# Kernel tuning notes

Measured on AMD Instinct MI355X. Metric: run time of the kernel, lower is better.

The kernel has to match this reference:

```python
import jax, jax.numpy as jnp
import numpy as np

N, E, F_IN, HID, EDIM = 20000, 320000, 16, 64, 1


def _add_self_loops(src, dst, eattr, n):
    # PyG add_self_loops with fill_value='mean': self-loop edge_attr = mean of
    # incoming edge_attr per destination node (0 if no incoming edges).
    deg = jax.ops.segment_sum(jnp.ones_like(eattr[:, 0]), dst, num_segments=n)
    mean_attr = jax.ops.segment_sum(eattr, dst, num_segments=n) / jnp.maximum(deg, 1.0)[:, None]
    loop = jnp.arange(n)
    return (jnp.concatenate([src, loop]), jnp.concatenate([dst, loop]),
            jnp.concatenate([eattr, mean_attr], axis=0))


def _gat_layer(x, src, dst, eattr, W, a_src, a_dst, We, a_e, b, heads, out_ch, n):
    # shared linear for src/dst (PyG GATConv with int in_channels)
    h = (x @ W).reshape(n, heads, out_ch)                      # [N,H,C]
    al_s = jnp.einsum('nhc,hc->nh', h, a_src)                  # [N,H]
    al_d = jnp.einsum('nhc,hc->nh', h, a_dst)
    ef = (eattr @ We).reshape(-1, heads, out_ch)               # [E,H,C]
    al_e = jnp.einsum('ehc,hc->eh', ef, a_e)                   # [E,H]
    alpha = jax.nn.leaky_relu(al_s[src] + al_d[dst] + al_e, 0.2)
    # segment softmax over destination node
    m = jax.ops.segment_max(alpha, dst, num_segments=n)
    m = jnp.where(jnp.isfinite(m), m, 0.0)
    ex = jnp.exp(alpha - m[dst])
    den = jax.ops.segment_sum(ex, dst, num_segments=n)
    coef = ex / (den[dst] + 1e-16)                             # [E,H]
    out = jax.ops.segment_sum(h[src] * coef[:, :, None], dst, num_segments=n)
    return out.reshape(n, heads * out_ch) + b


def setup_inputs() -> dict:
    key = jax.random.key(0)
    ks = jax.random.split(key, 24)
    s = 0.1
    inp = {
        'x': jax.random.normal(ks[0], (N, F_IN), jnp.float32),
        'edge_index': jax.random.randint(ks[1], (2, E), 0, N, jnp.int64),
        'edge_attr': jax.random.uniform(ks[2], (E, EDIM), jnp.float32),
        # layer 0: heads=4, in=16, out=64
        'W0': jax.random.normal(ks[3], (F_IN, 4 * HID), jnp.float32) * s,
        'as0': jax.random.normal(ks[4], (4, HID), jnp.float32) * s,
        'ad0': jax.random.normal(ks[5], (4, HID), jnp.float32) * s,
        'We0': jax.random.normal(ks[6], (EDIM, 4 * HID), jnp.float32) * s,
        'ae0': jax.random.normal(ks[7], (4, HID), jnp.float32) * s,
        'b0': jnp.zeros((4 * HID,), jnp.float32),
        # layer 1: heads=4, in=256, out=64
        'W1': jax.random.normal(ks[8], (4 * HID, 4 * HID), jnp.float32) * s,
        'as1': jax.random.normal(ks[9], (4, HID), jnp.float32) * s,
        'ad1': jax.random.normal(ks[10], (4, HID), jnp.float32) * s,
        'We1': jax.random.normal(ks[11], (EDIM, 4 * HID), jnp.float32) * s,
        'ae1': jax.random.normal(ks[12], (4, HID), jnp.float32) * s,
        'b1': jnp.zeros((4 * HID,), jnp.float32),
        # layer 2: heads=1, in=256, out=64
        'W2': jax.random.normal(ks[13], (4 * HID, HID), jnp.float32) * s,
        'as2': jax.random.normal(ks[14], (1, HID), jnp.float32) * s,
        'ad2': jax.random.normal(ks[15], (1, HID), jnp.float32) * s,
        'We2': jax.random.normal(ks[16], (EDIM, HID), jnp.float32) * s,
        'ae2': jax.random.normal(ks[17], (1, HID), jnp.float32) * s,
        'b2': jnp.zeros((HID,), jnp.float32),
        'ln_g': jnp.ones((HID,), jnp.float32),
        'ln_b': jnp.zeros((HID,), jnp.float32),
    }
    return inp


def reference(x, edge_index, edge_attr,
              W0, as0, ad0, We0, ae0, b0,
              W1, as1, ad1, We1, ae1, b1,
              W2, as2, ad2, We2, ae2, b2,
              ln_g, ln_b):
    n = x.shape[0]
    src, dst, eattr = _add_self_loops(edge_index[0], edge_index[1], edge_attr, n)
    h = _gat_layer(x, src, dst, eattr, W0, as0, ad0, We0, ae0, b0, 4, HID, n)
    h = jax.nn.elu(h)  # dropout is identity in eval
    h = _gat_layer(h, src, dst, eattr, W1, as1, ad1, We1, ae1, b1, 4, HID, n)
    h = jax.nn.elu(h)
    h = _gat_layer(h, src, dst, eattr, W2, as2, ad2, We2, ae2, b2, 1, HID, n)
    mu = jnp.mean(h, axis=-1, keepdims=True)
    var = jnp.mean((h - mu) ** 2, axis=-1, keepdims=True)
    return (h - mu) / jnp.sqrt(var + 1e-5) * ln_g + ln_b
```

## Files before the change

### kernel.cpp

```cpp
#include <hip/hip_runtime.h>
#include <hip/hip_bf16.h>
#include <math.h>


typedef __attribute__((ext_vector_type(8))) short short8;
typedef __attribute__((ext_vector_type(4))) float float4v;

#define CAP 64

__device__ __forceinline__ float wave_sum(float v) {
#pragma unroll
  for (int off = 32; off > 0; off >>= 1) v += __shfl_xor(v, off, 64);
  return v;
}

__device__ __forceinline__ unsigned short f2bf(float v) {
  unsigned u = __float_as_uint(v);
  unsigned r = u + 0x7fff + ((u >> 16) & 1);
  return (unsigned short)(r >> 16);
}

__device__ __forceinline__ float bf2f(unsigned short u) {
  return __uint_as_float(((unsigned)u) << 16);
}

__device__ __forceinline__ float sel4(float a, float b, float c, float d, int i) {
  return (i == 0) ? a : (i == 1) ? b : (i == 2) ? c : d;
}

__global__ __launch_bounds__(256) void k1_kernel(
    const float* __restrict__ x, const int* __restrict__ srcv, const int* __restrict__ dstv,
    const float* __restrict__ eattr,
    const float* __restrict__ W0, const float* __restrict__ as0, const float* __restrict__ ad0,
    const float* __restrict__ We0, const float* __restrict__ ae0,
    const float* __restrict__ W1, const float* __restrict__ as1, const float* __restrict__ ad1,
    const float* __restrict__ We1, const float* __restrict__ ae1,
    const float* __restrict__ W2, const float* __restrict__ as2, const float* __restrict__ ad2,
    const float* __restrict__ We2, const float* __restrict__ ae2,
    unsigned short* __restrict__ Wf1, unsigned short* __restrict__ Wf2,
    float* __restrict__ wedot, float* __restrict__ al0s, float* __restrict__ al0d,
    int* __restrict__ deg, int2* __restrict__ ebuf,
    int N, int E, int gD) {
  int b = blockIdx.x;
  int tid = threadIdx.x;
  if (b < 272) {
    int idx = b * 256 + tid;
    int j = idx & 7, lane = (idx >> 3) & 63, ks = (idx >> 9) & 7, nt = idx >> 12;
    int k = ks * 32 + (lane >> 4) * 8 + j;
    int col = lane & 15;
    float v = 0.f;
    if (nt < 16) {
      v = W1[(size_t)k * 256 + nt * 16 + col];
    } else if (col < 4) {
      for (int c = 0; c < 64; c++) v = fmaf(W1[(size_t)k * 256 + col * 64 + c], as1[col * 64 + c], v);
    } else if (col < 8) {
      int h = col - 4;
      for (int c = 0; c < 64; c++) v = fmaf(W1[(size_t)k * 256 + h * 64 + c], ad1[h * 64 + c], v);
    }
    Wf1[idx] = f2bf(v);
  } else if (b < 352) {
    int idx = (b - 272) * 256 + tid;
    int j = idx & 7, lane = (idx >> 3) & 63, ks = (idx >> 9) & 7, nt = idx >> 12;
    int k = ks * 32 + (lane >> 4) * 8 + j;
    int col = lane & 15;
    float v = 0.f;
    if (nt < 4) {
      v = W2[(size_t)k * 64 + nt * 16 + col];
    } else if (col < 1) {
      for (int c = 0; c < 64; c++) v = fmaf(W2[(size_t)k * 64 + c], as2[c], v);
    } else if (col < 2) {
      for (int c = 0; c < 64; c++) v = fmaf(W2[(size_t)k * 64 + c], ad2[c], v);
    }
    Wf2[idx] = f2bf(v);
  } else if (b == 352) {
    if (tid >= 64) return;
    int c = tid;
    for (int h = 0; h < 4; h++) {
      float v = wave_sum(We0[h * 64 + c] * ae0[h * 64 + c]);
      if (c == 0) wedot[h] = v;
    }
    for (int h = 0; h < 4; h++) {
      float v = wave_sum(We1[h * 64 + c] * ae1[h * 64 + c]);
      if (c == 0) wedot[4 + h] = v;
    }
    float v = wave_sum(We2[c] * ae2[c]);
    if (c == 0) wedot[8] = v;
  } else if (b < 353 + gD) {
    __shared__ float va[128];
    if (tid < 128) {
      int k = tid >> 3, col = tid & 7;
      float v = 0.f;
      if (col < 4) {
        for (int c = 0; c < 64; c++) v = fmaf(W0[(size_t)k * 256 + col * 64 + c], as0[col * 64 + c], v);
      } else {
        int h = col - 4;
        for (int c = 0; c < 64; c++) v = fmaf(W0[(size_t)k * 256 + h * 64 + c], ad0[h * 64 + c], v);
      }
      va[tid] = v;
    }
    __syncthreads();
    int node = (b - 353) * 256 + tid;
    if (node >= N) return;
    const float4* xr = (const float4*)(x + (size_t)node * 16);
    float4 xv[4];
#pragma unroll
    for (int q = 0; q < 4; q++) xv[q] = xr[q];
    float al[8];
#pragma unroll
    for (int j = 0; j < 8; j++) al[j] = 0.f;
#pragma unroll
    for (int k = 0; k < 16; k++) {
      float xk = ((const float*)xv)[k];
#pragma unroll
      for (int j = 0; j < 8; j++) al[j] = fmaf(xk, va[k * 8 + j], al[j]);
    }
    ((float4*)al0s)[node] = make_float4(al[0], al[1], al[2], al[3]);
    ((float4*)al0d)[node] = make_float4(al[4], al[5], al[6], al[7]);
  } else {
    int e = (b - 353 - gD) * 256 + tid;
    if (e >= E) return;
    int d = dstv[e];
    int s = srcv[e];
    float ea = eattr[e];
    int pos = atomicAdd(&deg[d], 1);
    if (pos < CAP) ebuf[(size_t)d * CAP + pos] = make_int2(s, __float_as_int(ea));
  }
}

__global__ __launch_bounds__(256) void fused0_kernel(
    const int* __restrict__ deg, const int2* __restrict__ ebuf,
    const float* __restrict__ al0s, const float* __restrict__ al0d,
    const float* __restrict__ wedot,
    const float* __restrict__ x, const float* __restrict__ W0,
    const float* __restrict__ b0, const unsigned short* __restrict__ Wf1,
    unsigned short* __restrict__ buf256, float* __restrict__ al1s,
    float* __restrict__ al1d, int n) {
  __shared__ unsigned short hrow[16][264];
  __shared__ float w0lds[4096];
  int tile = blockIdx.x;
  int wv = threadIdx.x >> 6;
  int lane = threadIdx.x & 63;
  int es = lane >> 4;
  int c = lane & 15;
  int le = lane >> 2;
  int lh = lane & 3;

#pragma unroll
  for (int i = 0; i < 4; i++) {
    int idx = i * 256 + threadIdx.x;
    ((float4*)w0lds)[idx] = ((const float4*)W0)[idx];
  }
  __syncthreads();

  for (int s = 0; s < 4; s++) {
    int r = wv * 4 + s;
    int node = tile * 16 + r;
    if (node < n) {
      int dg = deg[node];
      int cnt = dg < CAP ? dg : CAP;
      float xself = x[(size_t)node * 16 + c];
      float4 as4s = ((const float4*)al0s)[node];
      float4 ald4 = ((const float4*)al0d)[node];
      float aldP = sel4(ald4.x, ald4.y, ald4.z, ald4.w, lh);
      float wd0 = wedot[0], wd1 = wedot[1], wd2 = wedot[2], wd3 = wedot[3];
      float wdP = sel4(wd0, wd1, wd2, wd3, lh);

      float Z[4] = {0.f, 0.f, 0.f, 0.f};
      float denP = 0.f;
      float easumP = 0.f;

      for (int i = 0; i < cnt; i += 16) {
        int slot = i + le;
        bool av = slot < cnt;
        int2 re = ebuf[(size_t)node * CAP + slot];
        int srcE = av ? re.x : 0;
        float ev = av ? __int_as_float(re.y) : 0.f;
        int srcK[4];
        float xvK[4];
#pragma unroll
        for (int k = 0; k < 4; k++) srcK[k] = __shfl(srcE, (k * 4 + es) * 4, 64);
#pragma unroll
        for (int k = 0; k < 4; k++) xvK[k] = x[(size_t)srcK[k] * 16 + c];
        float a = al0s[(size_t)srcE * 4 + lh] + aldP + ev * wdP;
        a = fmaxf(a, 0.2f * a);
        a = fminf(a, 30.f);
        float wE = av ? __expf(a) : 0.f;
        denP += wE;
        easumP += (lh == 0) ? ev : 0.f;
#pragma unroll
        for (int k = 0; k < 4; k++) {
          int e4 = (k * 4 + es) * 4;
          float w0v = __shfl(wE, e4 + 0, 64);
          float w1v = __shfl(wE, e4 + 1, 64);
          float w2v = __shfl(wE, e4 + 2, 64);
          float w3v = __shfl(wE, e4 + 3, 64);
          Z[0] = fmaf(w0v, xvK[k], Z[0]);
          Z[1] = fmaf(w1v, xvK[k], Z[1]);
          Z[2] = fmaf(w2v, xvK[k], Z[2]);
          Z[3] = fmaf(w3v, xvK[k], Z[3]);
        }
      }

#pragma unroll
      for (int h = 0; h < 4; h++) {
        Z[h] += __shfl_xor(Z[h], 16, 64);
        Z[h] += __shfl_xor(Z[h], 32, 64);
      }
      denP += __shfl_xor(denP, 4, 64);
      denP += __shfl_xor(denP, 8, 64);
      denP += __shfl_xor(denP, 16, 64);
      denP += __shfl_xor(denP, 32, 64);
      float easum = wave_sum(easumP);

      float dsel = __shfl(denP, es, 64);
      float evs = easum / fmaxf((float)dg, 1.f);
      float as_e = sel4(as4s.x, as4s.y, as4s.z, as4s.w, es);
      float ald_e = sel4(ald4.x, ald4.y, ald4.z, ald4.w, es);
      float wd_e = sel4(wd0, wd1, wd2, wd3, es);
      float aS = as_e + ald_e + evs * wd_e;
      aS = fmaxf(aS, 0.2f * aS);
      aS = fminf(aS, 30.f);
      float wvs = __expf(aS);
      dsel += wvs;
      float zsel = sel4(Z[0], Z[1], Z[2], Z[3], es) + wvs * xself;
      float zn = zsel / (dsel + 1e-16f);

      float zc[16];
      int basel = lane & 48;
#pragma unroll
      for (int cc = 0; cc < 16; cc++) zc[cc] = __shfl(zn, basel + cc, 64);
      float o[4];
      float4 b4 = ((const float4*)b0)[lane];
#pragma unroll
      for (int jj = 0; jj < 4; jj++) o[jj] = ((const float*)&b4)[jj];
#pragma unroll
      for (int cc = 0; cc < 16; cc++) {
        float4 w0r = *(const float4*)&w0lds[cc * 256 + lane * 4];
#pragma unroll
        for (int jj = 0; jj < 4; jj++) o[jj] = fmaf(zc[cc], ((const float*)&w0r)[jj], o[jj]);
      }
      ushort4 o4;
      float ox = o[0] > 0.f ? o[0] : expm1f(o[0]);
      float oy = o[1] > 0.f ? o[1] : expm1f(o[1]);
      float oz = o[2] > 0.f ? o[2] : expm1f(o[2]);
      float ow = o[3] > 0.f ? o[3] : expm1f(o[3]);
      o4.x = f2bf(ox);
      o4.y = f2bf(oy);
      o4.z = f2bf(oz);
      o4.w = f2bf(ow);
      *(ushort4*)&hrow[r][lane * 4] = o4;
    } else {
      *(ushort4*)&hrow[r][lane * 4] = make_ushort4(0, 0, 0, 0);
    }
  }
  __syncthreads();

  int m = lane & 15, q = lane >> 4;
  int row0 = tile * 16;
  short8 afrag[8];
#pragma unroll
  for (int ks = 0; ks < 8; ks++) afrag[ks] = *(short8*)&hrow[m][ks * 32 + q * 8];

  const short8* wf = (const short8*)Wf1;
  for (int nt = wv; nt < 17; nt += 4) {
    const short8* bl = wf + (size_t)nt * 8 * 64 + lane;
    short8 bf[8];
#pragma unroll
    for (int ks = 0; ks < 8; ks++) bf[ks] = bl[ks * 64];
    float4v acc = {0.f, 0.f, 0.f, 0.f};
#pragma unroll
    for (int ks = 0; ks < 8; ks++)
      acc = __builtin_amdgcn_mfma_f32_16x16x32_bf16(afrag[ks], bf[ks], acc, 0, 0, 0);
    if (nt < 16) {
      int col = nt * 16 + m;
#pragma unroll
      for (int reg = 0; reg < 4; reg++) {
        int rr = row0 + q * 4 + reg;
        if (rr < n) buf256[(size_t)rr * 256 + col] = f2bf(acc[reg]);
      }
    } else {
#pragma unroll
      for (int reg = 0; reg < 4; reg++) {
        int rr = row0 + q * 4 + reg;
        if (rr < n) {
          if (m < 4) al1s[(size_t)rr * 4 + m] = acc[reg];
          else if (m < 8) al1d[(size_t)rr * 4 + (m - 4)] = acc[reg];
        }
      }
    }
  }
}

__global__ __launch_bounds__(256) void fused1_kernel(
    const int* __restrict__ deg, const int2* __restrict__ ebuf,
    const float* __restrict__ al1s, const float* __restrict__ al1d,
    const float* __restrict__ wedot,
    const unsigned short* __restrict__ buf256, const float* __restrict__ b1,
    const unsigned short* __restrict__ Wf2, unsigned short* __restrict__ buf64,
    float* __restrict__ al2s, float* __restrict__ al2d, int n) {
  __shared__ unsigned short hrow[16][264];
  int tile = blockIdx.x;
  int wv = threadIdx.x >> 6;
  int lane = threadIdx.x & 63;
  int half = lane >> 5;
  int l = lane & 31;
  int h4 = l >> 3;
  int le = lane >> 2;
  int lh = lane & 3;
  int eA0 = half ? 1 : 0;
  int eB0 = half ? 3 : 2;

  for (int s = 0; s < 4; s++) {
    int r = wv * 4 + s;
    int node = tile * 16 + r;
    if (node < n) {
      int dg = deg[node];
      int cnt = dg < CAP ? dg : CAP;
      float aldh = al1d[(size_t)node * 4 + h4];
      float alsh = al1s[(size_t)node * 4 + h4];
      float wdh = wedot[4 + h4];
      float aldP = al1d[(size_t)node * 4 + lh];
      float wdP = wedot[4 + lh];
      short8 rowS = ((const short8*)(buf256 + (size_t)node * 256))[l];

      float acc[8];
#pragma unroll
      for (int j = 0; j < 8; j++) acc[j] = 0.f;
      float denP = 0.f;
      float easumP = 0.f;

      for (int i = 0; i < cnt; i += 16) {
        int slot = i + le;
        bool av = slot < cnt;
        int2 re = ebuf[(size_t)node * CAP + slot];
        int srcE = av ? re.x : 0;
        float ev = av ? __int_as_float(re.y) : 0.f;
        int srcA[4], srcB[4];
#pragma unroll
        for (int k = 0; k < 4; k++) {
          srcA[k] = __shfl(srcE, (k * 4 + eA0) * 4, 64);
          srcB[k] = __shfl(srcE, (k * 4 + eB0) * 4, 64);
        }
        short8 rowA[4], rowB[4];
#pragma unroll
        for (int k = 0; k < 4; k++) {
          rowA[k] = ((const short8*)(buf256 + (size_t)srcA[k] * 256))[l];
          rowB[k] = ((const short8*)(buf256 + (size_t)srcB[k] * 256))[l];
        }
        float a = al1s[(size_t)srcE * 4 + lh] + aldP + ev * wdP;
        a = fmaxf(a, 0.2f * a);
        a = fminf(a, 30.f);
        float wE = av ? __expf(a) : 0.f;
        denP += wE;
        easumP += (lh == 0) ? ev : 0.f;
#pragma unroll
        for (int k = 0; k < 4; k++) {
          float wA = __shfl(wE, (k * 4 + eA0) * 4 + h4, 64);
          float wB = __shfl(wE, (k * 4 + eB0) * 4 + h4, 64);
          const unsigned short* pa = (const unsigned short*)&rowA[k];
          const unsigned short* pb = (const unsigned short*)&rowB[k];
#pragma unroll
          for (int j = 0; j < 8; j++) acc[j] = fmaf(wA, bf2f(pa[j]), acc[j]);
#pragma unroll
          for (int j = 0; j < 8; j++) acc[j] = fmaf(wB, bf2f(pb[j]), acc[j]);
        }
      }

#pragma unroll
      for (int j = 0; j < 8; j++) acc[j] += __shfl_xor(acc[j], 32, 64);
      denP += __shfl_xor(denP, 4, 64);
      denP += __shfl_xor(denP, 8, 64);
      denP += __shfl_xor(denP, 16, 64);
      denP += __shfl_xor(denP, 32, 64);
      float easum = wave_sum(easumP);
      float den = __shfl(denP, h4, 64);

      {
        float evs = easum / fmaxf((float)dg, 1.f);
        float a = alsh + aldh + evs * wdh;
        a = fmaxf(a, 0.2f * a);
        a = fminf(a, 30.f);
        float wvv = __expf(a);
        const unsigned short* ps = (const unsigned short*)&rowS;
        den += wvv;
#pragma unroll
        for (int j = 0; j < 8; j++) acc[j] = fmaf(wvv, bf2f(ps[j]), acc[j]);
      }

      if (half == 0) {
        float inv = 1.f / (den + 1e-16f);
        float4 bb0 = ((const float4*)b1)[l * 2];
        float4 bb1 = ((const float4*)b1)[l * 2 + 1];
        unsigned short o8[8];
#pragma unroll
        for (int j = 0; j < 8; j++) {
          float bjv = (j < 4) ? ((const float*)&bb0)[j] : ((const float*)&bb1)[j - 4];
          float o = acc[j] * inv + bjv;
          o = o > 0.f ? o : expm1f(o);
          o8[j] = f2bf(o);
        }
        *(short8*)&hrow[r][l * 8] = *(short8*)o8;
      }
    } else if ((lane >> 5) == 0) {
      unsigned short z8[8] = {0, 0, 0, 0, 0, 0, 0, 0};
      *(short8*)&hrow[r][(lane & 31) * 8] = *(short8*)z8;
    }
  }
  __syncthreads();

  int m = lane & 15, q = lane >> 4;
  int row0 = tile * 16;
  short8 afrag[8];
#pragma unroll
  for (int ks = 0; ks < 8; ks++) afrag[ks] = *(short8*)&hrow[m][ks * 32 + q * 8];

  const short8* wf = (const short8*)Wf2;
  for (int nt = wv; nt < 5; nt += 4) {
    const short8* bl = wf + (size_t)nt * 8 * 64 + lane;
    short8 bf[8];
#pragma unroll
    for (int ks = 0; ks < 8; ks++) bf[ks] = bl[ks * 64];
    float4v acc = {0.f, 0.f, 0.f, 0.f};
#pragma unroll
    for (int ks = 0; ks < 8; ks++)
      acc = __builtin_amdgcn_mfma_f32_16x16x32_bf16(afrag[ks], bf[ks], acc, 0, 0, 0);
    if (nt < 4) {
      int col = nt * 16 + m;
#pragma unroll
      for (int reg = 0; reg < 4; reg++) {
        int rr = row0 + q * 4 + reg;
        if (rr < n) buf64[(size_t)rr * 64 + col] = f2bf(acc[reg]);
      }
    } else {
#pragma unroll
      for (int reg = 0; reg < 4; reg++) {
        int rr = row0 + q * 4 + reg;
        if (rr < n) {
          if (m < 1) al2s[rr] = acc[reg];
          else if (m < 2) al2d[rr] = acc[reg];
        }
      }
    }
  }
}

__global__ __launch_bounds__(256) void agg_ln_kernel(
    const int* __restrict__ deg, const int2* __restrict__ ebuf,
    const float* __restrict__ al2s, const float* __restrict__ al2d,
    const float* __restrict__ wedot,
    const unsigned short* __restrict__ B, const float* __restrict__ bias,
    const float* __restrict__ ln_g, const float* __restrict__ ln_b,
    float* __restrict__ out, int n) {
  int wv = threadIdx.x >> 6;
  int node = blockIdx.x * 4 + wv;
  if (node >= n) return;
  int lane = threadIdx.x & 63;
  int q = lane >> 4;
  int l = lane & 15;
  int le = lane & 15;
  int dg = deg[node];
  int cnt = dg < CAP ? dg : CAP;
  float ald = al2d[node];
  float als = al2s[node];
  float wd = wedot[0];
  ushort4 bvS = ((const ushort4*)(B + (size_t)node * 64))[l];

  float4 acc = make_float4(0.f, 0.f, 0.f, 0.f);
  float denP = 0.f;
  float easumP = 0.f;

  for (int i = 0; i < cnt; i += 16) {
    int slot = i + le;
    bool av = slot < cnt;
    int2 re = ebuf[(size_t)node * CAP + slot];
    int srcE = av ? re.x : 0;
    float ev = av ? __int_as_float(re.y) : 0.f;
    int srcK[4];
#pragma unroll
    for (int k = 0; k < 4; k++) srcK[k] = __shfl(srcE, k * 4 + q, 64);
    ushort4 bvK[4];
#pragma unroll
    for (int k = 0; k < 4; k++) bvK[k] = ((const ushort4*)(B + (size_t)srcK[k] * 64))[l];
    float a = al2s[srcE] + ald + ev * wd;
    a = fmaxf(a, 0.2f * a);
    a = fminf(a, 30.f);
    float wE = av ? __expf(a) : 0.f;
    denP += wE;
    easumP += ev;
#pragma unroll
    for (int k = 0; k < 4; k++) {
      float w = __shfl(wE, k * 4 + q, 64);
      acc.x = fmaf(w, bf2f(bvK[k].x), acc.x);
      acc.y = fmaf(w, bf2f(bvK[k].y), acc.y);
      acc.z = fmaf(w, bf2f(bvK[k].z), acc.z);
      acc.w = fmaf(w, bf2f(bvK[k].w), acc.w);
    }
  }

  acc.x += __shfl_xor(acc.x, 32, 64);
  acc.y += __shfl_xor(acc.y, 32, 64);
  acc.z += __shfl_xor(acc.z, 32, 64);
  acc.w += __shfl_xor(acc.w, 32, 64);
  acc.x += __shfl_xor(acc.x, 16, 64);
  acc.y += __shfl_xor(acc.y, 16, 64);
  acc.z += __shfl_xor(acc.z, 16, 64);
  acc.w += __shfl_xor(acc.w, 16, 64);
  float den = wave_sum(denP) * 0.25f;
  float easum = wave_sum(easumP) * 0.25f;

  {
    float evs = easum / fmaxf((float)dg, 1.f);
    float a = als + ald + evs * wd;
    a = fmaxf(a, 0.2f * a);
    a = fminf(a, 30.f);
    float wv2 = __expf(a);
    den += wv2;
    acc.x = fmaf(wv2, bf2f(bvS.x), acc.x);
    acc.y = fmaf(wv2, bf2f(bvS.y), acc.y);
    acc.z = fmaf(wv2, bf2f(bvS.z), acc.z);
    acc.w = fmaf(wv2, bf2f(bvS.w), acc.w);
  }

  float inv = 1.f / (den + 1e-16f);
  float4 b4 = ((const float4*)bias)[l];
  float4 o;
  o.x = acc.x * inv + b4.x;
  o.y = acc.y * inv + b4.y;
  o.z = acc.z * inv + b4.z;
  o.w = acc.w * inv + b4.w;
  float s = (o.x + o.y) + (o.z + o.w);
#pragma unroll
  for (int off = 1; off < 16; off <<= 1) s += __shfl_xor(s, off, 64);
  float mu = s * (1.f / 64.f);
  float dx = o.x - mu, dy = o.y - mu, dz = o.z - mu, dw = o.w - mu;
  float v = (dx * dx + dy * dy) + (dz * dz + dw * dw);
#pragma unroll
  for (int off = 1; off < 16; off <<= 1) v += __shfl_xor(v, off, 64);
  float rs = rsqrtf(v * (1.f / 64.f) + 1e-5f);
  if (q == 0) {
    float4 g4 = ((const float4*)ln_g)[l];
    float4 lb4 = ((const float4*)ln_b)[l];
    float4 rr;
    rr.x = dx * rs * g4.x + lb4.x;
    rr.y = dy * rs * g4.y + lb4.y;
    rr.z = dz * rs * g4.z + lb4.z;
    rr.w = dw * rs * g4.w + lb4.w;
    ((float4*)(out + (size_t)node * 64))[l] = rr;
  }
}

extern "C" void kernel_launch(void* const* d_in, const int* in_sizes, int n_in,
                              void* d_out, int out_size, void* d_ws, size_t ws_size,
                              hipStream_t stream) {
  const float* x = (const float*)d_in[0];
  const int* ei = (const int*)d_in[1];
  const float* eattr = (const float*)d_in[2];
  const float* W0 = (const float*)d_in[3];
  const float* as0 = (const float*)d_in[4];
  const float* ad0 = (const float*)d_in[5];
  const float* We0 = (const float*)d_in[6];
  const float* ae0 = (const float*)d_in[7];
  const float* b0 = (const float*)d_in[8];
  const float* W1 = (const float*)d_in[9];
  const float* as1 = (const float*)d_in[10];
  const float* ad1 = (const float*)d_in[11];
  const float* We1 = (const float*)d_in[12];
  const float* ae1 = (const float*)d_in[13];
  const float* b1 = (const float*)d_in[14];
  const float* W2 = (const float*)d_in[15];
  const float* as2 = (const float*)d_in[16];
  const float* ad2 = (const float*)d_in[17];
  const float* We2 = (const float*)d_in[18];
  const float* ae2 = (const float*)d_in[19];
  const float* b2 = (const float*)d_in[20];
  const float* lng = (const float*)d_in[21];
  const float* lnb = (const float*)d_in[22];
  float* outp = (float*)d_out;

  const int N = in_sizes[0] / 16;
  const int E = in_sizes[1] / 2;
  const int* srcv = ei;
  const int* dstv = ei + E;

  char* w = (char*)d_ws;
  size_t off = 0;
  auto alloc = [&](size_t bytes) -> void* {
    void* p = w + off;
    off += (bytes + 255) & ~(size_t)255;
    return p;
  };
  int* deg = (int*)alloc((size_t)N * 4);
  size_t zero_bytes = off;
  int2* ebuf = (int2*)alloc(((size_t)N * CAP + 16) * 8);
  float* wedot = (float*)alloc(16 * 4);
  float* al0s = (float*)alloc((size_t)N * 4 * 4);
  float* al0d = (float*)alloc((size_t)N * 4 * 4);
  float* al1s = (float*)alloc((size_t)N * 4 * 4);
  float* al1d = (float*)alloc((size_t)N * 4 * 4);
  float* al2s = (float*)alloc((size_t)N * 4);
  float* al2d = (float*)alloc((size_t)N * 4);
  unsigned short* Wf1 = (unsigned short*)alloc((size_t)17 * 4096 * 2);
  unsigned short* Wf2 = (unsigned short*)alloc((size_t)5 * 4096 * 2);
  unsigned short* buf256 = (unsigned short*)alloc((size_t)N * 256 * 2);
  unsigned short* buf64 = (unsigned short*)alloc((size_t)N * 64 * 2);
  (void)ws_size;

  hipMemsetAsync(d_ws, 0, zero_bytes, stream);

  int gE = (E + 255) / 256;
  int gD = (N + 255) / 256;

  k1_kernel<<<353 + gD + gE, 256, 0, stream>>>(
      x, srcv, dstv, eattr, W0, as0, ad0, We0, ae0, W1, as1, ad1, We1, ae1,
      W2, as2, ad2, We2, ae2, Wf1, Wf2, wedot, al0s, al0d, deg, ebuf, N, E, gD);

  int gT = (N + 15) / 16;
  int gNode4 = (N + 3) / 4;

  fused0_kernel<<<gT, 256, 0, stream>>>(deg, ebuf, al0s, al0d, wedot, x, W0, b0,
                                        Wf1, buf256, al1s, al1d, N);

  fused1_kernel<<<gT, 256, 0, stream>>>(deg, ebuf, al1s, al1d, wedot, buf256, b1,
                                        Wf2, buf64, al2s, al2d, N);

  agg_ln_kernel<<<gNode4, 256, 0, stream>>>(deg, ebuf, al2s, al2d, wedot + 8,
                                            buf64, b2, lng, lnb, outp, N);
}
```

Before: 210.6 us.

## Software-pipeline edge-list loads across chunks and nodes in GAT aggregation kernels

```diff
diff --git a/kernel.cpp b/kernel.cpp
--- a/kernel.cpp
+++ b/kernel.cpp
@@ -152,29 +152,81 @@
   }
   __syncthreads();
 
+  float wd0 = wedot[0], wd1 = wedot[1], wd2 = wedot[2], wd3 = wedot[3];
+  float wdP = sel4(wd0, wd1, wd2, wd3, lh);
+
+  int base0 = tile * 16 + wv * 4;
+  int dgA[4];
+#pragma unroll
+  for (int t = 0; t < 4; t++) {
+    int nd = base0 + t;
+    dgA[t] = deg[nd < n ? nd : n - 1];
+  }
+
+  int cnt0 = dgA[0] < CAP ? dgA[0] : CAP;
+  int nodeC = base0 < n ? base0 : n - 1;
+  int2 reC = ebuf[(size_t)nodeC * CAP + le];
+  bool avP = le < cnt0;
+  int srcEP = avP ? reC.x : 0;
+  float evP = avP ? __int_as_float(reC.y) : 0.f;
+  int srcKP[4];
+  float xvKP[4];
+#pragma unroll
+  for (int k = 0; k < 4; k++) srcKP[k] = __shfl(srcEP, (k * 4 + es) * 4, 64);
+#pragma unroll
+  for (int k = 0; k < 4; k++) xvKP[k] = x[(size_t)srcKP[k] * 16 + c];
+  float alvP = al0s[(size_t)srcEP * 4 + lh];
+
   for (int s = 0; s < 4; s++) {
     int r = wv * 4 + s;
     int node = tile * 16 + r;
     if (node < n) {
-      int dg = deg[node];
+      int dg = dgA[s];
       int cnt = dg < CAP ? dg : CAP;
+      int nextNode = node + 1 < n ? node + 1 : n - 1;
+      int cntN = (s < 3) ? (dgA[s + 1] < CAP ? dgA[s + 1] : CAP) : 0;
       float xself = x[(size_t)node * 16 + c];
       float4 as4s = ((const float4*)al0s)[node];
       float4 ald4 = ((const float4*)al0d)[node];
       float aldP = sel4(ald4.x, ald4.y, ald4.z, ald4.w, lh);
-      float wd0 = wedot[0], wd1 = wedot[1], wd2 = wedot[2], wd3 = wedot[3];
-      float wdP = sel4(wd0, wd1, wd2, wd3, lh);
 
       float Z[4] = {0.f, 0.f, 0.f, 0.f};
       float denP = 0.f;
       float easumP = 0.f;
 
-      for (int i = 0; i < cnt; i += 16) {
+      {
+        size_t naddr = (16 < cnt) ? (size_t)node * CAP + 16 + le
+                                  : (size_t)nextNode * CAP + le;
+        int2 reN = ebuf[naddr];
+        float a = alvP + aldP + evP * wdP;
+        a = fmaxf(a, 0.2f * a);
+        a = fminf(a, 30.f);
+        float wE = avP ? __expf(a) : 0.f;
+        denP += wE;
+        easumP += (lh == 0) ? evP : 0.f;
+#pragma unroll
+        for (int k = 0; k < 4; k++) {
+          int e4 = (k * 4 + es) * 4;
+          float w0v = __shfl(wE, e4 + 0, 64);
+          float w1v = __shfl(wE, e4 + 1, 64);
+          float w2v = __shfl(wE, e4 + 2, 64);
+          float w3v = __shfl(wE, e4 + 3, 64);
+          Z[0] = fmaf(w0v, xvKP[k], Z[0]);
+          Z[1] = fmaf(w1v, xvKP[k], Z[1]);
+          Z[2] = fmaf(w2v, xvKP[k], Z[2]);
+          Z[3] = fmaf(w3v, xvKP[k], Z[3]);
+        }
+        reC = reN;
+      }
+
+      for (int i = 16; i < cnt; i += 16) {
+        size_t naddr = (i + 16 < cnt) ? (size_t)node * CAP + i + 16 + le
+                                      : (size_t)nextNode * CAP + le;
+        int2 reN = ebuf[naddr];
         int slot = i + le;
         bool av = slot < cnt;
-        int2 re = ebuf[(size_t)node * CAP + slot];
-        int srcE = av ? re.x : 0;
-        float ev = av ? __int_as_float(re.y) : 0.f;
+        int srcE = av ? reC.x : 0;
+        float ev = av ? __int_as_float(reC.y) : 0.f;
         int srcK[4];
         float xvK[4];
 #pragma unroll
@@ -199,6 +251,19 @@
           Z[2] = fmaf(w2v, xvK[k], Z[2]);
           Z[3] = fmaf(w3v, xvK[k], Z[3]);
         }
+        reC = reN;
+      }
+
+      {
+        bool av2 = le < cntN;
+        int srcE2 = av2 ? reC.x : 0;
+        avP = av2;
+        evP = av2 ? __int_as_float(reC.y) : 0.f;
+#pragma unroll
+        for (int k = 0; k < 4; k++) srcKP[k] = __shfl(srcE2, (k * 4 + es) * 4, 64);
+#pragma unroll
+        for (int k = 0; k < 4; k++) xvKP[k] = x[(size_t)srcKP[k] * 16 + c];
+        alvP = al0s[(size_t)srcE2 * 4 + lh];
       }
 
 #pragma unroll
@@ -310,17 +375,42 @@
   int eA0 = half ? 1 : 0;
   int eB0 = half ? 3 : 2;
 
+  float wdh = wedot[4 + h4];
+  float wdP = wedot[4 + lh];
+
+  int base0 = tile * 16 + wv * 4;
+  int dgA[4];
+#pragma unroll
+  for (int t = 0; t < 4; t++) {
+    int nd = base0 + t;
+    dgA[t] = deg[nd < n ? nd : n - 1];
+  }
+
+  int cnt0 = dgA[0] < CAP ? dgA[0] : CAP;
+  int nodeC = base0 < n ? base0 : n - 1;
+  int2 reC = ebuf[(size_t)nodeC * CAP + le];
+  bool avP = le < cnt0;
+  int srcEP = avP ? reC.x : 0;
+  float evP = avP ? __int_as_float(reC.y) : 0.f;
+  int srcAP[4], srcBP[4];
+#pragma unroll
+  for (int k = 0; k < 4; k++) {
+    srcAP[k] = __shfl(srcEP, (k * 4 + eA0) * 4, 64);
+    srcBP[k] = __shfl(srcEP, (k * 4 + eB0) * 4, 64);
+  }
+  float alvP = al1s[(size_t)srcEP * 4 + lh];
+
   for (int s = 0; s < 4; s++) {
     int r = wv * 4 + s;
     int node = tile * 16 + r;
     if (node < n) {
-      int dg = deg[node];
+      int dg = dgA[s];
       int cnt = dg < CAP ? dg : CAP;
+      int nextNode = node + 1 < n ? node + 1 : n - 1;
+      int cntN = (s < 3) ? (dgA[s + 1] < CAP ? dgA[s + 1] : CAP) : 0;
       float aldh = al1d[(size_t)node * 4 + h4];
       float alsh = al1s[(size_t)node * 4 + h4];
-      float wdh = wedot[4 + h4];
       float aldP = al1d[(size_t)node * 4 + lh];
-      float wdP = wedot[4 + lh];
       short8 rowS = ((const short8*)(buf256 + (size_t)node * 256))[l];
 
       float acc[8];
@@ -329,12 +419,44 @@
       float denP = 0.f;
       float easumP = 0.f;
 
-      for (int i = 0; i < cnt; i += 16) {
+      {
+        size_t naddr = (16 < cnt) ? (size_t)node * CAP + 16 + le
+                                  : (size_t)nextNode * CAP + le;
+        int2 reN = ebuf[naddr];
+        short8 rowA[4], rowB[4];
+#pragma unroll
+        for (int k = 0; k < 4; k++) {
+          rowA[k] = ((const short8*)(buf256 + (size_t)srcAP[k] * 256))[l];
+          rowB[k] = ((const short8*)(buf256 + (size_t)srcBP[k] * 256))[l];
+        }
+        float a = alvP + aldP + evP * wdP;
+        a = fmaxf(a, 0.2f * a);
+        a = fminf(a, 30.f);
+        float wE = avP ? __expf(a) : 0.f;
+        denP += wE;
+        easumP += (lh == 0) ? evP : 0.f;
+#pragma unroll
+        for (int k = 0; k < 4; k++) {
+          float wA = __shfl(wE, (k * 4 + eA0) * 4 + h4, 64);
+          float wB = __shfl(wE, (k * 4 + eB0) * 4 + h4, 64);
+          const unsigned short* pa = (const unsigned short*)&rowA[k];
+          const unsigned short* pb = (const unsigned short*)&rowB[k];
+#pragma unroll
+          for (int j = 0; j < 8; j++) acc[j] = fmaf(wA, bf2f(pa[j]), acc[j]);
+#pragma unroll
+          for (int j = 0; j < 8; j++) acc[j] = fmaf(wB, bf2f(pb[j]), acc[j]);
+        }
+        reC = reN;
+      }
+
+      for (int i = 16; i < cnt; i += 16) {
+        size_t naddr = (i + 16 < cnt) ? (size_t)node * CAP + i + 16 + le
+                                      : (size_t)nextNode * CAP + le;
+        int2 reN = ebuf[naddr];
         int slot = i + le;
         bool av = slot < cnt;
-        int2 re = ebuf[(size_t)node * CAP + slot];
-        int srcE = av ? re.x : 0;
-        float ev = av ? __int_as_float(re.y) : 0.f;
+        int srcE = av ? reC.x : 0;
+        float ev = av ? __int_as_float(reC.y) : 0.f;
         int srcA[4], srcB[4];
 #pragma unroll
         for (int k = 0; k < 4; k++) {
@@ -364,6 +486,20 @@
 #pragma unroll
           for (int j = 0; j < 8; j++) acc[j] = fmaf(wB, bf2f(pb[j]), acc[j]);
         }
+        reC = reN;
+      }
+
+      {
+        bool av2 = le < cntN;
+        int srcE2 = av2 ? reC.x : 0;
+        avP = av2;
+        evP = av2 ? __int_as_float(reC.y) : 0.f;
+#pragma unroll
+        for (int k = 0; k < 4; k++) {
+          srcAP[k] = __shfl(srcE2, (k * 4 + eA0) * 4, 64);
+          srcBP[k] = __shfl(srcE2, (k * 4 + eB0) * 4, 64);
+        }
+        alvP = al1s[(size_t)srcE2 * 4 + lh];
       }
 
 #pragma unroll
@@ -401,9 +537,9 @@
         }
         *(short8*)&hrow[r][l * 8] = *(short8*)o8;
       }
-    } else if ((lane >> 5) == 0) {
+    } else if (half == 0) {
       unsigned short z8[8] = {0, 0, 0, 0, 0, 0, 0, 0};
-      *(short8*)&hrow[r][(lane & 31) * 8] = *(short8*)z8;
+      *(short8*)&hrow[r][l * 8] = *(short8*)z8;
     }
   }
   __syncthreads();
```

Result: no change. 209.9 us (-0.3%).
